# Performance work log

Measured on AMD Instinct MI355X. Metric: run time of the kernel, lower is better.

## Reference

```python
import jax, jax.numpy as jnp
import numpy as np

B, S, D = 2, 2048, 1024
H, DH = 16, 64  # n_heads, d_head = d_model // n_heads


def setup_inputs() -> dict:
    key = jax.random.key(0)
    ks = jax.random.split(key, 8)
    sc = lambda d: 1.0 / np.sqrt(d)
    return {
        "x": jax.random.normal(ks[0], (B, S, D), jnp.float32),
        "context": jax.random.normal(ks[1], (B, D), jnp.float32),
        "prev_state": jax.random.normal(ks[2], (B, S, D), jnp.float32),
        "attention_mask": jnp.ones((B, 1, S, S), dtype=bool),
        "Wq": jax.random.normal(ks[3], (D, D), jnp.float32) * sc(D),
        "Wk": jax.random.normal(ks[4], (D, D), jnp.float32) * sc(D),
        "Wv": jax.random.normal(ks[5], (D, D), jnp.float32) * sc(D),
        "Wo": jax.random.normal(ks[6], (D, D), jnp.float32) * sc(D),
        "Wc": jax.random.normal(ks[7], (D, DH), jnp.float32) * sc(D),
        "alpha": jnp.ones((1,), jnp.float32),
        "beta": jnp.ones((1,), jnp.float32),
    }


def reference(x, context, prev_state, attention_mask, Wq, Wk, Wv, Wo, Wc, alpha, beta):
    b, s, d = x.shape
    # projections (Linear with no bias, weight stored as [out, in] -> x @ W.T)
    q = (x @ Wq.T).reshape(b, s, H, DH).transpose(0, 2, 1, 3)  # (B,H,S,DH)
    k = (x @ Wk.T).reshape(b, s, H, DH).transpose(0, 2, 1, 3)
    v = (x @ Wv.T).reshape(b, s, H, DH).transpose(0, 2, 1, 3)

    inv_sqrt_dh = 1.0 / jnp.sqrt(jnp.asarray(DH, x.dtype))
    scores = jnp.einsum("bhqd,bhkd->bhqk", q, k) * inv_sqrt_dh

    # CFM: context-flow matching bias, rank-1 per-pair term from global context
    c = context @ Wc  # (B, DH)
    qc = jnp.einsum("bhqd,bd->bhq", q, c)
    kc = jnp.einsum("bhkd,bd->bhk", k, c)
    cfm = qc[..., :, None] * kc[..., None, :] / DH  # (B,H,S,S)

    # AFM: anti-flow matching bias from previous layer state (first d_head dims)
    p = prev_state[..., :DH]  # (B,S,DH)
    afm = jnp.einsum("bhqd,bkd->bhqk", q, p) * inv_sqrt_dh

    scores = scores + alpha[0] * cfm - beta[0] * afm
    scores = jnp.where(attention_mask, scores, jnp.asarray(-1e9, scores.dtype))

    w = jax.nn.softmax(scores, axis=-1)
    out = jnp.einsum("bhqk,bhkd->bhqd", w, v)  # (B,H,S,DH)
    out = out.transpose(0, 2, 1, 3).reshape(b, s, d)
    return out @ Wo.T
```

## Files before the change

kernel.cpp:

```cpp
#include <hip/hip_runtime.h>
#include <stdint.h>

#define D_  1024
#define S_  2048
#define B_  2
#define H_  16
#define DH_ 64
#define M_  (B_*S_)

typedef __bf16 bf16x8 __attribute__((ext_vector_type(8)));
typedef float  f32x4  __attribute__((ext_vector_type(4)));
typedef float  f32x16 __attribute__((ext_vector_type(16)));
typedef short  short8 __attribute__((ext_vector_type(8)));
typedef unsigned uint4v __attribute__((ext_vector_type(4)));
typedef unsigned short u16;

static __device__ __forceinline__ u16 f2bf(float f){
  union { float f; unsigned u; } v; v.f = f;
  unsigned r = v.u + 0x7FFF + ((v.u >> 16) & 1);
  return (u16)(r >> 16);
}
static __device__ __forceinline__ f32x4 mfma16(short8 a, short8 b, f32x4 c){
  return __builtin_amdgcn_mfma_f32_16x16x32_bf16(
      __builtin_bit_cast(bf16x8, a), __builtin_bit_cast(bf16x8, b), c, 0, 0, 0);
}
static __device__ __forceinline__ f32x16 mfma32(short8 a, short8 b, f32x16 c){
  return __builtin_amdgcn_mfma_f32_32x32x16_bf16(
      __builtin_bit_cast(bf16x8, a), __builtin_bit_cast(bf16x8, b), c, 0, 0, 0);
}
static __device__ __forceinline__ f32x16 zero16(){
  f32x16 z = {0,0,0,0,0,0,0,0,0,0,0,0,0,0,0,0};
  return z;
}
static __device__ __forceinline__ float fexp2(float x){
#if __has_builtin(__builtin_amdgcn_exp2f)
  return __builtin_amdgcn_exp2f(x);
#else
  return __exp2f(x);
#endif
}
static __device__ __forceinline__ unsigned cvtpk(float lo, float hi){
  unsigned r;
  asm("v_cvt_pk_bf16_f32 %0, %1, %2" : "=v"(r) : "v"(lo), "v"(hi));
  return r;
}
static __device__ __forceinline__ void gl_lds16(const u16* g, u16* lds){
  __builtin_amdgcn_global_load_lds(
      (const __attribute__((address_space(1))) void*)(uintptr_t)g,
      (__attribute__((address_space(3))) void*)(uintptr_t)lds, 16, 0, 0);
}

__global__ void k_f2bf(const float* __restrict__ in, u16* __restrict__ out, int n4){
  int i = blockIdx.x * blockDim.x + threadIdx.x;
  if(i >= n4) return;
  float4 v = ((const float4*)in)[i];
  ushort4 o; o.x = f2bf(v.x); o.y = f2bf(v.y); o.z = f2bf(v.z); o.w = f2bf(v.w);
  ((ushort4*)out)[i] = o;
}

__global__ void k_f2bf4(const float* __restrict__ a0, const float* __restrict__ a1,
                        const float* __restrict__ a2, const float* __restrict__ a3,
                        u16* __restrict__ o0, u16* __restrict__ o1,
                        u16* __restrict__ o2, u16* __restrict__ o3, int n4){
  const float* in; u16* out;
  switch(blockIdx.y){
    case 0: in=a0; out=o0; break;
    case 1: in=a1; out=o1; break;
    case 2: in=a2; out=o2; break;
    default: in=a3; out=o3; break;
  }
  int i = blockIdx.x * blockDim.x + threadIdx.x;
  if(i >= n4) return;
  float4 v = ((const float4*)in)[i];
  ushort4 o; o.x = f2bf(v.x); o.y = f2bf(v.y); o.z = f2bf(v.z); o.w = f2bf(v.w);
  ((ushort4*)out)[i] = o;
}

__global__ void k_ctx(const float* __restrict__ context, const float* __restrict__ Wc,
                      float* __restrict__ cvec, int* __restrict__ flags){
  __shared__ float partial[4][2][64];
  int t = threadIdx.x;
  if(t < 2) flags[t] = 1;
  int c = t >> 7;
  int b = (t >> 6) & 1;
  int j = t & 63;
  float s = 0.f;
  #pragma unroll 8
  for(int d = c*256; d < (c+1)*256; ++d) s += context[b*D_ + d] * Wc[d*DH_ + j];
  partial[c][b][j] = s;
  __syncthreads();
  if(t < 128){
    int b2 = t >> 6, j2 = t & 63;
    cvec[b2*DH_ + j2] = partial[0][b2][j2] + partial[1][b2][j2]
                      + partial[2][b2][j2] + partial[3][b2][j2];
  }
}

__global__ void k_mask_check(const uint4* __restrict__ m, int n16, int* flags){
  int i = blockIdx.x * blockDim.x + threadIdx.x;
  bool ok8 = true, ok32 = true;
  if(i < n16){
    uint4 v = m[i];
    ok8  = (v.x==0x01010101u)&&(v.y==0x01010101u)&&(v.z==0x01010101u)&&(v.w==0x01010101u);
    ok32 = (v.x==1u)&&(v.y==1u)&&(v.z==1u)&&(v.w==1u);
  }
  unsigned long long b8  = __ballot(!ok8);
  unsigned long long b32 = __ballot(!ok32);
  if((threadIdx.x & 63) == 0){
    if(b8)  flags[0] = 0;
    if(b32) flags[1] = 0;
  }
}

__global__ __launch_bounds__(256,3) void k_gemm_qkv(const u16* __restrict__ A,
    const u16* __restrict__ Wcat, u16* __restrict__ Qb, u16* __restrict__ Kb,
    u16* __restrict__ VT, const float* __restrict__ cvec,
    const float* __restrict__ prev, const float* __restrict__ beta_p,
    float* __restrict__ qcb, float* __restrict__ kcb){
  __shared__ u16 As[128*64];
  __shared__ u16 Bs[128*64];
  __shared__ float red[2][2][64];
  const int tid = threadIdx.x;
  const int w = tid >> 6, l = tid & 63;
  const int wr = w >> 1, wc = w & 1;
  const int id = blockIdx.x;
  const int bn = id >> 5;
  const int bm = id & 31;
  const int lr = l & 15, lh = l >> 4;
  const int srow = l >> 3, scol = (l & 7) * 8;

  f32x4 acc[4][4] = {};

  for(int kt = 0; kt < 16; ++kt){
    const int k0 = kt * 64;
    #pragma unroll
    for(int i = 0; i < 4; ++i){
      const int chunk = i*4 + w;
      gl_lds16(A    + (size_t)(bm*128 + chunk*8 + srow)*D_ + k0 + scol, &As[chunk*512]);
      gl_lds16(Wcat + (size_t)(bn*128 + chunk*8 + srow)*D_ + k0 + scol, &Bs[chunk*512]);
    }
    __syncthreads();
    #pragma unroll
    for(int kk = 0; kk < 2; ++kk){
      short8 a[4], b[4];
      #pragma unroll
      for(int m = 0; m < 4; ++m)
        a[m] = *(const short8*)&As[(wr*64 + m*16 + lr)*64 + kk*32 + lh*8];
      #pragma unroll
      for(int n = 0; n < 4; ++n)
        b[n] = *(const short8*)&Bs[(wc*64 + n*16 + lr)*64 + kk*32 + lh*8];
      #pragma unroll
      for(int m = 0; m < 4; ++m)
        #pragma unroll
        for(int n = 0; n < 4; ++n)
          acc[m][n] = mfma16(a[m], b[n], acc[m][n]);
    }
    __syncthreads();
  }

  const int b = bm >> 4;

  if(bn < 16){
    float cv[4];
    #pragma unroll
    for(int n = 0; n < 4; ++n) cv[n] = cvec[b*DH_ + n*16 + lr];
    float part[4][4];
    #pragma unroll
    for(int m = 0; m < 4; ++m)
      #pragma unroll
      for(int r = 0; r < 4; ++r){
        float p = acc[m][0][r]*cv[0] + acc[m][1][r]*cv[1]
                + acc[m][2][r]*cv[2] + acc[m][3][r]*cv[3];
        p += __shfl_xor(p, 1, 64); p += __shfl_xor(p, 2, 64);
        p += __shfl_xor(p, 4, 64); p += __shfl_xor(p, 8, 64);
        part[m][r] = p;
      }
    if(lr == 0){
      #pragma unroll
      for(int m = 0; m < 4; ++m)
        #pragma unroll
        for(int r = 0; r < 4; ++r)
          red[wr][wc][m*16 + lh*4 + r] = part[m][r];
    }
    __syncthreads();
    {
      int wr2 = tid >> 7, wc2 = (tid >> 6) & 1, i = tid & 63;
      int s = (bm & 15)*128 + wr2*64 + i;
      int head = (bn & 7)*2 + wc2;
      float* qkc = (bn < 8) ? qcb : kcb;
      qkc[((size_t)b*H_ + head)*S_ + s] = red[wr2][wc2][i];
    }
  }

  if(bn < 8){
    #pragma unroll
    for(int m = 0; m < 4; ++m){
      const size_t row0 = (size_t)bm*128 + wr*64 + m*16 + lh*4;
      #pragma unroll
      for(int n = 0; n < 4; ++n){
        const size_t col = (size_t)bn*128 + wc*64 + n*16 + lr;
        #pragma unroll
        for(int r = 0; r < 4; ++r)
          Qb[(row0 + r)*D_ + col] = f2bf(acc[m][n][r]);
      }
    }
  } else if(bn < 16){
    const float beta = beta_p[0];
    const float KSCALE = 0.125f * 1.44269504088896340736f;
    #pragma unroll
    for(int m = 0; m < 4; ++m){
      const size_t row0 = (size_t)bm*128 + wr*64 + m*16 + lh*4;
      #pragma unroll
      for(int n = 0; n < 4; ++n){
        const size_t col = (size_t)(bn - 8)*128 + wc*64 + n*16 + lr;
        #pragma unroll
        for(int r = 0; r < 4; ++r){
          float v = (acc[m][n][r] - beta * prev[(row0 + r)*D_ + n*16 + lr]) * KSCALE;
          Kb[(row0 + r)*D_ + col] = f2bf(v);
        }
      }
    }
  } else {
    #pragma unroll
    for(int m = 0; m < 4; ++m){
      const int s0 = (bm & 15)*128 + wr*64 + m*16 + lh*4;
      #pragma unroll
      for(int n = 0; n < 4; ++n){
        const int col = (bn - 16)*128 + wc*64 + n*16 + lr;
        ushort4 o;
        o.x = f2bf(acc[m][n][0]); o.y = f2bf(acc[m][n][1]);
        o.z = f2bf(acc[m][n][2]); o.w = f2bf(acc[m][n][3]);
        *(ushort4*)&VT[((size_t)(b*1024 + col))*S_ + s0] = o;
      }
    }
  }
}

__global__ __launch_bounds__(256,2) void k_gemm_o(const u16* __restrict__ A,
    const u16* __restrict__ W, float* __restrict__ Cout){
  __shared__ u16 As[128*64];
  __shared__ u16 Bs[64*64];
  const int tid = threadIdx.x;
  const int w = tid >> 6, l = tid & 63;
  const int wr = w >> 1, wc = w & 1;
  const int bm = blockIdx.x >> 4;
  const int bn = blockIdx.x & 15;
  const int lr = l & 15, lh = l >> 4;
  const int srow = l >> 3, scol = (l & 7) * 8;

  f32x4 acc[4][2] = {};

  for(int kt = 0; kt < 16; ++kt){
    const int k0 = kt * 64;
    #pragma unroll
    for(int i = 0; i < 4; ++i){
      const int chunk = i*4 + w;
      gl_lds16(A + (size_t)(bm*128 + chunk*8 + srow)*D_ + k0 + scol, &As[chunk*512]);
    }
    #pragma unroll
    for(int i = 0; i < 2; ++i){
      const int chunk = w*2 + i;
      gl_lds16(W + (size_t)(bn*64 + chunk*8 + srow)*D_ + k0 + scol, &Bs[chunk*512]);
    }
    __syncthreads();
    #pragma unroll
    for(int kk = 0; kk < 2; ++kk){
      short8 a[4], b[2];
      #pragma unroll
      for(int m = 0; m < 4; ++m)
        a[m] = *(const short8*)&As[(wr*64 + m*16 + lr)*64 + kk*32 + lh*8];
      #pragma unroll
      for(int n = 0; n < 2; ++n)
        b[n] = *(const short8*)&Bs[(wc*32 + n*16 + lr)*64 + kk*32 + lh*8];
      #pragma unroll
      for(int m = 0; m < 4; ++m)
        #pragma unroll
        for(int n = 0; n < 2; ++n)
          acc[m][n] = mfma16(a[m], b[n], acc[m][n]);
    }
    __syncthreads();
  }
  #pragma unroll
  for(int m = 0; m < 4; ++m){
    const size_t row0 = (size_t)bm*128 + wr*64 + m*16 + lh*4;
    #pragma unroll
    for(int n = 0; n < 2; ++n){
      const size_t col = (size_t)bn*64 + wc*32 + n*16 + lr;
      #pragma unroll
      for(int r = 0; r < 4; ++r)
        Cout[(row0 + r)*D_ + col] = acc[m][n][r];
    }
  }
}

template<bool AM>
__device__ __forceinline__ void attn_1w(
    const u16* __restrict__ Kb_h, const u16* __restrict__ VT_h,
    const float* __restrict__ kcp, const unsigned char* __restrict__ maskr,
    u16* __restrict__ KB, const short8 (&qa)[4], float aq,
    f32x16 (&oacc)[2], float& lp,
    int q32, int hi, int hb, int srow, int sdh, int xk){
  short8 vfA[2][4], vfB[2][4];

  #define STGK(T, BUF) { _Pragma("unroll") for(int j = 0; j < 8; ++j)            \
      gl_lds16(Kb_h + (size_t)((T)*64 + j*8 + srow)*D_ + sdh,                    \
               KB + (BUF)*4096 + j*512); }
  #define LOADV(T, VF) { _Pragma("unroll") for(int d2 = 0; d2 < 2; ++d2){        \
      _Pragma("unroll") for(int c = 0; c < 4; ++c)                               \
        VF[d2][c] = *(const short8*)&VT_h[(size_t)(d2*32 + q32)*S_               \
                                          + (size_t)(T)*64 + c*16 + hb]; } }

  STGK(0, 0);
  LOADV(0, vfA);

  #define BODY(T, BUF, VCUR, VNXT) {                                             \
    if((T) < 31){                                                                \
      STGK((T)+1, (BUF)^1);                                                      \
      LOADV((T)+1, VNXT);                                                        \
      asm volatile("s_waitcnt vmcnt(16)" ::: "memory");                          \
    } else {                                                                     \
      asm volatile("s_waitcnt vmcnt(0)" ::: "memory");                           \
    }                                                                            \
    const int k0 = (T)*64;                                                       \
    unsigned pk[2][8];                                                           \
    _Pragma("unroll") for(int kg = 0; kg < 2; ++kg){                             \
      f32x16 sacc = zero16();                                                    \
      _Pragma("unroll") for(int c = 0; c < 4; ++c){                              \
        short8 kf = *(const short8*)&KB[(BUF)*4096 + (kg*32 + q32)*64            \
                                        + ((c*16 + hb) ^ xk)];                   \
        sacc = mfma32(kf, qa[c], sacc);                                          \
      }                                                                          \
      float p[16];                                                               \
      _Pragma("unroll") for(int rg = 0; rg < 4; ++rg){                           \
        f32x4 kv = *(const f32x4*)&kcp[k0 + kg*32 + rg*8 + hi*4];                \
        unsigned mu = 0x01010101u;                                               \
        if(AM) mu = *(const unsigned*)&maskr[k0 + kg*32 + rg*8 + hi*4];          \
        _Pragma("unroll") for(int j = 0; j < 4; ++j){                            \
          float tv = sacc[rg*4 + j] + aq*kv[j];                                  \
          if(AM){ if(((mu >> (8*j)) & 255u) == 0u) tv = -160.0f; }               \
          float e = fexp2(tv);                                                   \
          lp += e; p[rg*4 + j] = e;                                              \
        }                                                                        \
      }                                                                          \
      _Pragma("unroll") for(int i = 0; i < 8; ++i)                               \
        pk[kg][i] = cvtpk(p[2*i], p[2*i+1]);                                     \
    }                                                                            \
    _Pragma("unroll") for(int c = 0; c < 4; ++c){                                \
      const int kg = c >> 1, c4 = (c & 1)*4;                                     \
      unsigned x0 = pk[kg][c4+0], y0 = pk[kg][c4+2];                             \
      unsigned x1 = pk[kg][c4+1], y1 = pk[kg][c4+3];                             \
      asm("v_permlane32_swap_b32 %0, %1" : "+v"(x0), "+v"(y0));                  \
      asm("v_permlane32_swap_b32 %0, %1" : "+v"(x1), "+v"(y1));                  \
      uint4v pb = {x0, x1, y0, y1};                                              \
      short8 pbf = __builtin_bit_cast(short8, pb);                               \
      _Pragma("unroll") for(int d2 = 0; d2 < 2; ++d2)                            \
        oacc[d2] = mfma32(VCUR[d2][c], pbf, oacc[d2]);                           \
    }                                                                            \
  }

  for(int t2 = 0; t2 < 16; ++t2){
    BODY(2*t2,   0, vfA, vfB);
    BODY(2*t2+1, 1, vfB, vfA);
  }
  #undef BODY
  #undef LOADV
  #undef STGK
}

__global__ __launch_bounds__(64,2) void k_attn(const u16* __restrict__ Qb,
    const u16* __restrict__ Kb, const u16* __restrict__ VT,
    const float* __restrict__ qc, const float* __restrict__ kc,
    const float* __restrict__ alpha_p, const unsigned char* __restrict__ mask,
    const int* __restrict__ flags, u16* __restrict__ Ob){
  __shared__ u16 Kbuf[2][4096];
  const int l = threadIdx.x;
  const int q32 = l & 31, hi = l >> 5, hb = hi*8;
  const int id = blockIdx.x;
  const int bh = id & 31, qb = id >> 5;
  const int b = bh >> 4, h = bh & 15;
  const int q0 = qb*32;
  const float aL = alpha_p[0] * (1.0f/64.0f) * 1.44269504088896340736f;
  const bool allones = (flags[0] | flags[1]) != 0;
  const u16* Kb_h = Kb + (size_t)b*S_*D_ + h*DH_;
  const u16* VT_h = VT + ((size_t)(b*1024 + h*DH_))*S_;
  const float* kcp = kc + (size_t)bh*S_;
  const unsigned char* maskr = mask + ((size_t)b*S_ + q0 + q32)*S_;

  const int srow = l >> 3;
  const int sdh  = ((l & 7) ^ srow) * 8;
  const int xk   = (q32 & 7) << 3;

  short8 qa[4];
  #pragma unroll
  for(int c = 0; c < 4; ++c)
    qa[c] = *(const short8*)&Qb[((size_t)b*S_ + q0 + q32)*D_ + h*DH_ + c*16 + hb];
  const float aq = aL * qc[(size_t)bh*S_ + q0 + q32];

  f32x16 oacc[2] = {zero16(), zero16()};
  float lp = 0.f;

  if(allones)
    attn_1w<false>(Kb_h, VT_h, kcp, maskr, &Kbuf[0][0], qa, aq, oacc, lp,
                   q32, hi, hb, srow, sdh, xk);
  else
    attn_1w<true>(Kb_h, VT_h, kcp, maskr, &Kbuf[0][0], qa, aq, oacc, lp,
                  q32, hi, hb, srow, sdh, xk);

  float lt = lp + __shfl_xor(lp, 32, 64);
  float inv = 1.0f / lt;
  u16* orow = Ob + ((size_t)b*S_ + q0 + q32)*D_ + h*DH_;
  #pragma unroll
  for(int dh2 = 0; dh2 < 2; ++dh2)
    #pragma unroll
    for(int rg = 0; rg < 4; ++rg){
      ushort4 o;
      o.x = f2bf(oacc[dh2][rg*4+0]*inv);
      o.y = f2bf(oacc[dh2][rg*4+1]*inv);
      o.z = f2bf(oacc[dh2][rg*4+2]*inv);
      o.w = f2bf(oacc[dh2][rg*4+3]*inv);
      *(ushort4*)&orow[dh2*32 + rg*8 + hi*4] = o;
    }
}

extern "C" void kernel_launch(void* const* d_in, const int* in_sizes, int n_in,
                              void* d_out, int out_size, void* d_ws, size_t ws_size,
                              hipStream_t stream){
  const float* x    = (const float*)d_in[0];
  const float* ctx  = (const float*)d_in[1];
  const float* prev = (const float*)d_in[2];
  const unsigned char* mask = (const unsigned char*)d_in[3];
  const float* Wq = (const float*)d_in[4];
  const float* Wk = (const float*)d_in[5];
  const float* Wv = (const float*)d_in[6];
  const float* Wo = (const float*)d_in[7];
  const float* Wc = (const float*)d_in[8];
  const float* alpha = (const float*)d_in[9];
  const float* beta  = (const float*)d_in[10];

  char* ws = (char*)d_ws;
  size_t off = 0;
  auto alloc = [&](size_t bytes)->void*{
    void* p = ws + off; off += (bytes + 255) & ~(size_t)255; return p;
  };
  u16* xb   = (u16*)alloc((size_t)M_*D_*2);
  u16* wcat = (u16*)alloc((size_t)3*D_*D_*2);
  u16* wob  = (u16*)alloc((size_t)D_*D_*2);
  u16* Qb   = (u16*)alloc((size_t)M_*D_*2);
  u16* Kb   = (u16*)alloc((size_t)M_*D_*2);
  u16* VT   = (u16*)alloc((size_t)B_*D_*S_*2);
  float* qcb  = (float*)alloc((size_t)B_*H_*S_*4);
  float* kcb  = (float*)alloc((size_t)B_*H_*S_*4);
  float* cvec = (float*)alloc(512);
  int*  flags = (int*)alloc(64);
  u16* Ob = xb;

  k_f2bf<<<M_*D_/4/256, 256, 0, stream>>>(x, xb, M_*D_/4);
  {
    dim3 g(D_*D_/4/256, 4);
    k_f2bf4<<<g, 256, 0, stream>>>(Wq, Wk, Wv, Wo,
        wcat, wcat + (size_t)D_*D_, wcat + (size_t)2*D_*D_, wob, D_*D_/4);
  }
  k_ctx<<<1, 512, 0, stream>>>(ctx, Wc, cvec, flags);
  {
    int n16 = B_*S_*S_/16;
    k_mask_check<<<n16/256, 256, 0, stream>>>((const uint4*)mask, n16, flags);
  }
  k_gemm_qkv<<<768, 256, 0, stream>>>(xb, wcat, Qb, Kb, VT, cvec, prev, beta, qcb, kcb);
  k_attn<<<2048, 64, 0, stream>>>(Qb, Kb, VT, qcb, kcb, alpha, mask, flags, Ob);
  k_gemm_o<<<512, 256, 0, stream>>>(Ob, wob, (float*)d_out);
}
```

Measured before the change: 180.6 us.

## Share K tile staging across two waves per attention block

The attention kernel moves from one wave per 32-query block to two waves per block covering 64 queries, with each wave staging half of the shared K tile into LDS. Every K tile loaded from global memory is therefore reused by twice as many queries, roughly halving K traffic. In exchange, workgroup barriers replace the explicit vmcnt waits, which may reduce the overlap between loads and compute. The launch bounds change to 128 threads with 3 blocks per CU, and the grid is halved.

```diff
diff --git a/kernel.cpp b/kernel.cpp
--- a/kernel.cpp
+++ b/kernel.cpp
@@ -294,17 +294,18 @@
 }
 
 template<bool AM>
-__device__ __forceinline__ void attn_1w(
+__device__ __forceinline__ void attn_v9(
     const u16* __restrict__ Kb_h, const u16* __restrict__ VT_h,
     const float* __restrict__ kcp, const unsigned char* __restrict__ maskr,
     u16* __restrict__ KB, const short8 (&qa)[4], float aq,
     f32x16 (&oacc)[2], float& lp,
-    int q32, int hi, int hb, int srow, int sdh, int xk){
+    int q32, int hi, int hb, int srow, int sdh, int wv, int xk){
   short8 vfA[2][4], vfB[2][4];
 
-  #define STGK(T, BUF) { _Pragma("unroll") for(int j = 0; j < 8; ++j)            \
-      gl_lds16(Kb_h + (size_t)((T)*64 + j*8 + srow)*D_ + sdh,                    \
-               KB + (BUF)*4096 + j*512); }
+  #define STGK(T, BUF) { _Pragma("unroll") for(int j = 0; j < 4; ++j){           \
+      const int ck = j*2 + wv;                                                   \
+      gl_lds16(Kb_h + (size_t)((T)*64 + ck*8 + srow)*D_ + sdh,                   \
+               KB + (BUF)*4096 + ck*512); } }
   #define LOADV(T, VF) { _Pragma("unroll") for(int d2 = 0; d2 < 2; ++d2){        \
       _Pragma("unroll") for(int c = 0; c < 4; ++c)                               \
         VF[d2][c] = *(const short8*)&VT_h[(size_t)(d2*32 + q32)*S_               \
@@ -312,15 +313,10 @@
 
   STGK(0, 0);
   LOADV(0, vfA);
+  __syncthreads();
 
   #define BODY(T, BUF, VCUR, VNXT) {                                             \
-    if((T) < 31){                                                                \
-      STGK((T)+1, (BUF)^1);                                                      \
-      LOADV((T)+1, VNXT);                                                        \
-      asm volatile("s_waitcnt vmcnt(16)" ::: "memory");                          \
-    } else {                                                                     \
-      asm volatile("s_waitcnt vmcnt(0)" ::: "memory");                           \
-    }                                                                            \
+    if((T) < 31){ STGK((T)+1, (BUF)^1); LOADV((T)+1, VNXT); }                    \
     const int k0 = (T)*64;                                                       \
     unsigned pk[2][8];                                                           \
     _Pragma("unroll") for(int kg = 0; kg < 2; ++kg){                             \
@@ -356,6 +352,7 @@
       _Pragma("unroll") for(int d2 = 0; d2 < 2; ++d2)                            \
         oacc[d2] = mfma32(VCUR[d2][c], pbf, oacc[d2]);                           \
     }                                                                            \
+    __syncthreads();                                                             \
   }
 
   for(int t2 = 0; t2 < 16; ++t2){
@@ -367,24 +364,25 @@
   #undef STGK
 }
 
-__global__ __launch_bounds__(64,2) void k_attn(const u16* __restrict__ Qb,
+__global__ __launch_bounds__(128,3) void k_attn(const u16* __restrict__ Qb,
     const u16* __restrict__ Kb, const u16* __restrict__ VT,
     const float* __restrict__ qc, const float* __restrict__ kc,
     const float* __restrict__ alpha_p, const unsigned char* __restrict__ mask,
     const int* __restrict__ flags, u16* __restrict__ Ob){
   __shared__ u16 Kbuf[2][4096];
-  const int l = threadIdx.x;
+  const int tid = threadIdx.x;
+  const int wv = tid >> 6, l = tid & 63;
   const int q32 = l & 31, hi = l >> 5, hb = hi*8;
   const int id = blockIdx.x;
   const int bh = id & 31, qb = id >> 5;
   const int b = bh >> 4, h = bh & 15;
-  const int q0 = qb*32;
+  const int q0w = qb*64 + wv*32;
   const float aL = alpha_p[0] * (1.0f/64.0f) * 1.44269504088896340736f;
   const bool allones = (flags[0] | flags[1]) != 0;
   const u16* Kb_h = Kb + (size_t)b*S_*D_ + h*DH_;
   const u16* VT_h = VT + ((size_t)(b*1024 + h*DH_))*S_;
   const float* kcp = kc + (size_t)bh*S_;
-  const unsigned char* maskr = mask + ((size_t)b*S_ + q0 + q32)*S_;
+  const unsigned char* maskr = mask + ((size_t)b*S_ + q0w + q32)*S_;
 
   const int srow = l >> 3;
   const int sdh  = ((l & 7) ^ srow) * 8;
@@ -393,22 +391,22 @@
   short8 qa[4];
   #pragma unroll
   for(int c = 0; c < 4; ++c)
-    qa[c] = *(const short8*)&Qb[((size_t)b*S_ + q0 + q32)*D_ + h*DH_ + c*16 + hb];
-  const float aq = aL * qc[(size_t)bh*S_ + q0 + q32];
+    qa[c] = *(const short8*)&Qb[((size_t)b*S_ + q0w + q32)*D_ + h*DH_ + c*16 + hb];
+  const float aq = aL * qc[(size_t)bh*S_ + q0w + q32];
 
   f32x16 oacc[2] = {zero16(), zero16()};
   float lp = 0.f;
 
   if(allones)
-    attn_1w<false>(Kb_h, VT_h, kcp, maskr, &Kbuf[0][0], qa, aq, oacc, lp,
-                   q32, hi, hb, srow, sdh, xk);
+    attn_v9<false>(Kb_h, VT_h, kcp, maskr, &Kbuf[0][0], qa, aq, oacc, lp,
+                   q32, hi, hb, srow, sdh, wv, xk);
   else
-    attn_1w<true>(Kb_h, VT_h, kcp, maskr, &Kbuf[0][0], qa, aq, oacc, lp,
-                  q32, hi, hb, srow, sdh, xk);
+    attn_v9<true>(Kb_h, VT_h, kcp, maskr, &Kbuf[0][0], qa, aq, oacc, lp,
+                  q32, hi, hb, srow, sdh, wv, xk);
 
   float lt = lp + __shfl_xor(lp, 32, 64);
   float inv = 1.0f / lt;
-  u16* orow = Ob + ((size_t)b*S_ + q0 + q32)*D_ + h*DH_;
+  u16* orow = Ob + ((size_t)b*S_ + q0w + q32)*D_ + h*DH_;
   #pragma unroll
   for(int dh2 = 0; dh2 < 2; ++dh2)
     #pragma unroll
@@ -466,6 +464,6 @@
     k_mask_check<<<n16/256, 256, 0, stream>>>((const uint4*)mask, n16, flags);
   }
   k_gemm_qkv<<<768, 256, 0, stream>>>(xb, wcat, Qb, Kb, VT, cvec, prev, beta, qcb, kcb);
-  k_attn<<<2048, 64, 0, stream>>>(Qb, Kb, VT, qcb, kcb, alpha, mask, flags, Ob);
+  k_attn<<<1024, 128, 0, stream>>>(Qb, Kb, VT, qcb, kcb, alpha, mask, flags, Ob);
   k_gemm_o<<<512, 256, 0, stream>>>(Ob, wob, (float*)d_out);
 }
```

Result: slower. 194.7 us (+7.8%).
